# Kernel optimization log

Hardware: AMD Instinct MI355X
Metric: run time of the kernel (lower is better)

Reference implementation:

```python
import jax, jax.numpy as jnp
import numpy as np

# Module hyperparameters (init_kwargs)
KH, KW = 1, 1            # kernel_size
PATCH_H, PATCH_W = 21, 21  # patch_size (displacement grid)
SH, SW = 1, 1            # stride
PAD_H, PAD_W = 0, 0      # padding
DILP_H, DILP_W = 1, 1    # dilation_patch
B, C, H, W = 8, 256, 64, 96


def setup_inputs() -> dict:
    key = jax.random.key(0)
    k1, k2 = jax.random.split(key)
    input1 = jax.random.normal(k1, (B, C, H, W), dtype=jnp.float32)
    input2 = jax.random.normal(k2, (B, C, H, W), dtype=jnp.float32)
    return {"input1": input1, "input2": input2}


def _correlation(x1, x2):
    """FlowNet-style spatial correlation (cost volume).

    out[b, pi, pj, i, j] = sum_{c, ki, kj}
        x1_pad[b, c, i*SH + ki, j*SW + kj] *
        x2_pad[b, c, i*SH + ki + (pi - radH)*DILP_H, j*SW + kj + (pj - radW)*DILP_W]
    Out-of-bounds reads of x2 are zero (handled by padding).
    """
    radH, radW = PATCH_H // 2, PATCH_W // 2
    x1p = jnp.pad(x1, ((0, 0), (0, 0), (PAD_H, PAD_H), (PAD_W, PAD_W)))
    x2p = jnp.pad(x2, ((0, 0), (0, 0),
                       (PAD_H + radH * DILP_H, PAD_H + radH * DILP_H),
                       (PAD_W + radW * DILP_W, PAD_W + radW * DILP_W)))
    Hp, Wp = H + 2 * PAD_H, W + 2 * PAD_W
    oH = (Hp - KH) // SH + 1
    oW = (Wp - KW) // SW + 1

    # displacement grid -> start offsets into x2p (0 corresponds to -rad shift)
    sh = jnp.arange(PATCH_H, dtype=jnp.int32) * DILP_H
    sw = jnp.arange(PATCH_W, dtype=jnp.int32) * DILP_W
    starts = jnp.stack(jnp.meshgrid(sh, sw, indexing="ij"), axis=-1).reshape(-1, 2)

    def step(carry, s):
        # shifted view of x2 aligned with padded x1
        sl = jax.lax.dynamic_slice(x2p, (0, 0, s[0], s[1]), (B, C, Hp, Wp))
        prod = jnp.sum(x1p * sl, axis=1)  # [B, Hp, Wp], channel reduction
        # kernel-window sum + output stride (KH=KW=1 -> single strided slice)
        acc = jnp.zeros((B, oH, oW), dtype=prod.dtype)
        for ki in range(KH):
            for kj in range(KW):
                acc = acc + jax.lax.slice(
                    prod, (0, ki, kj),
                    (B, ki + (oH - 1) * SH + 1, kj + (oW - 1) * SW + 1),
                    (1, SH, SW))
        return carry, acc

    _, out = jax.lax.scan(step, None, starts)  # [PATCH_H*PATCH_W, B, oH, oW]
    out = out.reshape(PATCH_H, PATCH_W, B, oH, oW)
    return jnp.transpose(out, (2, 0, 1, 3, 4))  # [B, patchH, patchW, oH, oW]


def reference(input1, input2):
    return _correlation(input1, input2)
```

## Files before the change

kernel.cpp:

```cpp
#include <hip/hip_runtime.h>

typedef __attribute__((ext_vector_type(8))) short short8;
typedef __attribute__((ext_vector_type(4))) float f32x4;
typedef __attribute__((ext_vector_type(4))) unsigned short us4;

constexpr int NB = 8, NC = 256, IH = 64, IW = 96;
constexpr int PATCH = 21, RAD = 10;
constexpr int TI = 8, TJ = 8;
constexpr int WIN = 28, NWIN = 784;
constexpr int KC = 32, NKS = NC / KC;
constexpr int PLANE = IH * IW;
constexpr int PH = IH + 2 * RAD, PW = IW + 2 * RAD;
constexpr int NBCH = NWIN * 4;
constexpr int NCHUNK = NBCH + 256;
constexpr int ASTR = IH * IW * KC;
constexpr int BSTR = PH * PW * KC;
constexpr size_t X1T_ELEMS = (size_t)NB * NKS * ASTR;
constexpr size_t X2P_ELEMS = (size_t)NB * NKS * BSTR;
constexpr int GSTR = 65;

__device__ __forceinline__ unsigned short f2bf(float f) {
  unsigned u = __builtin_bit_cast(unsigned, f);
  u += 0x7fffu + ((u >> 16) & 1u);
  return (unsigned short)(u >> 16);
}

__global__ __launch_bounds__(256) void x1_to_kmajor(
    const float* __restrict__ src, unsigned short* __restrict__ dst) {
  __shared__ float lsf[32 * 97];
  const int blk = blockIdx.x;
  const int ct = blk & 7, i = (blk >> 3) & 63, b = blk >> 9;
  const int c0 = ct * 32, t = threadIdx.x;
  const float* sp = src + ((size_t)b * NC + c0) * PLANE + (size_t)i * IW;
#pragma unroll
  for (int k = 0; k < 12; ++k) {
    int idx = k * 256 + t;
    int c = idx / 96, j = idx - c * 96;
    lsf[c * 97 + j] = sp[(size_t)c * PLANE + j];
  }
  __syncthreads();
  unsigned short* dp = dst + (((size_t)(b * NKS + ct) * IH + i) * IW) * KC;
#pragma unroll
  for (int k = 0; k < 3; ++k) {
    int o = k * 256 + t;
    int j = o >> 3, cq = o & 7;
    us4 v = {f2bf(lsf[(cq * 4 + 0) * 97 + j]), f2bf(lsf[(cq * 4 + 1) * 97 + j]),
             f2bf(lsf[(cq * 4 + 2) * 97 + j]), f2bf(lsf[(cq * 4 + 3) * 97 + j])};
    *(us4*)&dp[(size_t)j * KC + cq * 4] = v;
  }
}

__global__ __launch_bounds__(256) void x2_to_kmajor_pad(
    const float* __restrict__ src, unsigned short* __restrict__ dst) {
  __shared__ float lsf[32 * 97];
  const int blk = blockIdx.x;
  const int ct = blk & 7, i = (blk >> 3) % PH, b = blk / (PH * 8);
  const int c0 = ct * 32, t = threadIdx.x;
  const int isrc = i - RAD;
  const bool rowok = (unsigned)isrc < (unsigned)IH;
  if (rowok) {
    const float* sp = src + ((size_t)b * NC + c0) * PLANE + (size_t)isrc * IW;
#pragma unroll
    for (int k = 0; k < 12; ++k) {
      int idx = k * 256 + t;
      int c = idx / 96, j = idx - c * 96;
      lsf[c * 97 + j] = sp[(size_t)c * PLANE + j];
    }
  }
  __syncthreads();
  unsigned short* dp = dst + (((size_t)(b * NKS + ct) * PH + i) * PW) * KC;
#pragma unroll
  for (int k = 0; k < 4; ++k) {
    int o = k * 256 + t;
    if (o < PW * 8) {
      int j = o >> 3, cq = o & 7;
      int jsrc = j - RAD;
      us4 v = {0, 0, 0, 0};
      if (rowok && (unsigned)jsrc < (unsigned)IW)
        v = us4{f2bf(lsf[(cq * 4 + 0) * 97 + jsrc]), f2bf(lsf[(cq * 4 + 1) * 97 + jsrc]),
                f2bf(lsf[(cq * 4 + 2) * 97 + jsrc]), f2bf(lsf[(cq * 4 + 3) * 97 + jsrc])};
      *(us4*)&dp[(size_t)j * KC + cq * 4] = v;
    }
  }
}

__global__ __launch_bounds__(512, 2) void corr_pipe8(
    const unsigned short* __restrict__ x1k, const unsigned short* __restrict__ x2k,
    float* __restrict__ out) {
  __shared__ __attribute__((aligned(16))) unsigned short ls[3 * NCHUNK * 8];

  const int t = threadIdx.x, lane = t & 63, wv = t >> 6;
  const int bid = blockIdx.x;
  const int b = bid & 7;
  const int tile = bid >> 3;
  const int ti = tile / 12, tj = tile - ti * 12;
  const int i0 = ti * TI, j0 = tj * TJ;
  const int cbeg = 6 * wv;
  const int qk = lane >> 4, lr = lane & 15;

  const unsigned short* x1b = x1k + (size_t)b * NKS * ASTR;
  const unsigned short* x2b = x2k + (size_t)b * NKS * BSTR;

  const unsigned short* srcp[7];
#pragma unroll
  for (int it = 0; it < 7; ++it) {
    int q = it * 512 + t;
    if (q < NBCH) {
      int w = ((q >> 3) << 1) | (((q >> 2) ^ (q >> 4)) & 1);
      int c4 = (q & 3) ^ (w & 3);
      int wi = w / WIN, wj = w - wi * WIN;
      srcp[it] = x2b + ((size_t)(i0 + wi) * PW + (j0 + wj)) * KC + c4 * 8;
    } else {
      int qa = (q - NBCH) & 255;
      int m = ((qa >> 3) << 1) | (((qa >> 2) ^ (qa >> 4)) & 1);
      int c4 = (qa & 3) ^ (m & 3);
      srcp[it] = x1b + ((size_t)(i0 + (m >> 3)) * IW + (j0 + (m & 7))) * KC + c4 * 8;
    }
  }

  f32x4 acc[4][7];
#pragma unroll
  for (int a = 0; a < 4; ++a)
#pragma unroll
    for (int cc = 0; cc < 7; ++cc) acc[a][cc] = (f32x4){0.f, 0.f, 0.f, 0.f};

#define STAGE(BUF, KS)                                                              \
  {                                                                                 \
    unsigned short* lb = &ls[(BUF) * NCHUNK * 8];                                   \
    _Pragma("unroll")                                                               \
    for (int it = 0; it < 6; ++it)                                                  \
      __builtin_amdgcn_global_load_lds(                                             \
          (const void*)(srcp[it] + (size_t)(KS) * BSTR),                            \
          (void*)(lb + (it * 512 + wv * 64) * 8), 16, 0, 0);                        \
    if (wv < 5)                                                                     \
      __builtin_amdgcn_global_load_lds(                                             \
          (const void*)(srcp[6] + (size_t)(KS) * (wv == 0 ? BSTR : ASTR)),          \
          (void*)(lb + (3072 + wv * 64) * 8), 16, 0, 0);                            \
  }

#define COMPUTE(BUF)                                                                \
  {                                                                                 \
    const unsigned short* lb = &ls[(BUF) * NCHUNK * 8];                             \
    short8 af0 = *(const short8*)(lb + (NBCH + ((4 * (lr) + qk) ^ (lr & 7))) * 8);        \
    short8 af1 = *(const short8*)(lb + (NBCH + ((4 * (16 + lr) + qk) ^ (lr & 7))) * 8);   \
    short8 af2 = *(const short8*)(lb + (NBCH + ((4 * (32 + lr) + qk) ^ (lr & 7))) * 8);   \
    short8 af3 = *(const short8*)(lb + (NBCH + ((4 * (48 + lr) + qk) ^ (lr & 7))) * 8);   \
    _Pragma("unroll")                                                               \
    for (int cc = 0; cc < 7; ++cc) {                                                \
      int wrow = 16 * (cbeg + cc) + lr;                                             \
      int slot = (4 * wrow + qk) ^ (lr & 7);                                        \
      short8 bf = *(const short8*)(lb + slot * 8);                                  \
      acc[0][cc] = __builtin_amdgcn_mfma_f32_16x16x32_bf16(af0, bf, acc[0][cc], 0, 0, 0); \
      acc[1][cc] = __builtin_amdgcn_mfma_f32_16x16x32_bf16(af1, bf, acc[1][cc], 0, 0, 0); \
      acc[2][cc] = __builtin_amdgcn_mfma_f32_16x16x32_bf16(af2, bf, acc[2][cc], 0, 0, 0); \
      acc[3][cc] = __builtin_amdgcn_mfma_f32_16x16x32_bf16(af3, bf, acc[3][cc], 0, 0, 0); \
    }                                                                               \
  }

  STAGE(0, 0)
  STAGE(1, 1)

#define ITER(KS, VM)                                           \
  if ((KS) < 6) STAGE((KS + 2) % 3, KS + 2)                    \
  asm volatile("s_waitcnt vmcnt(" #VM ")" ::: "memory");       \
  asm volatile("s_barrier" ::: "memory");                      \
  COMPUTE(KS % 3)                                              \
  asm volatile("s_barrier" ::: "memory");

  ITER(0, 12)
  ITER(1, 12)
  ITER(2, 12)
  ITER(3, 12)
  ITER(4, 12)
  ITER(5, 12)
  ITER(6, 6)
  ITER(7, 0)
#undef ITER
#undef COMPUTE
#undef STAGE

  float* gf = (float*)ls;
#pragma unroll
  for (int ch = 0; ch < 2; ++ch) {
    __syncthreads();
    const int n0 = ch ? 384 : 0;
#pragma unroll
    for (int a = 0; a < 4; ++a)
#pragma unroll
      for (int cc = 0; cc < 7; ++cc) {
        int ccg = cbeg + cc;
        if (ch ? (ccg >= 24) : (ccg <= 24)) {
          int nl = 16 * ccg + lr - n0;
          int mb = 16 * a + 4 * qk;
          float* gp = &gf[nl * GSTR + mb];
          gp[0] = acc[a][cc][0]; gp[1] = acc[a][cc][1];
          gp[2] = acc[a][cc][2]; gp[3] = acc[a][cc][3];
        }
      }
    __syncthreads();
    for (int s = t; s < 1764; s += 512) {
      int pidx = s / 21, pj = s - pidx * 21;
      int ii = 0, rem = pidx, stop = 0;
#pragma unroll
      for (int k = 0; k < 7; ++k) {
        int cnt = ch ? (7 + k) : (14 - k);
        int go = (!stop) && (rem >= cnt);
        rem -= go ? cnt : 0;
        ii += go;
        stop |= !go;
      }
      int pi = ch ? (14 - ii + rem) : rem;
      int nl = 28 * (pi + ii) + pj - n0;
      int ms = 8 * ii;
      float g[8];
#pragma unroll
      for (int e = 0; e < 8; ++e) g[e] = gf[(nl + e) * GSTR + ms + e];
      float* op = out + ((((size_t)b * PATCH + pi) * PATCH + pj) * IH + (i0 + ii)) * IW + j0;
      f32x4 v0 = {g[0], g[1], g[2], g[3]};
      f32x4 v1 = {g[4], g[5], g[6], g[7]};
      *(f32x4*)op = v0;
      *(f32x4*)(op + 4) = v1;
    }
  }
}

constexpr int LDKF = 40;
__global__ __launch_bounds__(512, 2) void corr_mfma_fb(
    const float* __restrict__ x1, const float* __restrict__ x2, float* __restrict__ out) {
  __shared__ __attribute__((aligned(16))) unsigned short lsA[64 * LDKF];
  __shared__ __attribute__((aligned(16))) unsigned short lsB[NWIN * LDKF];
  const int t = threadIdx.x;
  const int b = blockIdx.y;
  const int ti = blockIdx.x / 12, tj = blockIdx.x % 12;
  const int i0 = ti * TI, j0 = tj * TJ;
  const int lane = t & 63, wv = t >> 6;
  const int mtp = wv >> 2, cg = wv & 3, cbeg = cg * 12;
  const int qk = lane >> 4, lr = lane & 15;
  f32x4 acc[2][13];
#pragma unroll
  for (int a = 0; a < 2; ++a)
#pragma unroll
    for (int cc = 0; cc < 13; ++cc) acc[a][cc] = (f32x4){0.f, 0.f, 0.f, 0.f};
  const int am = t & 63, ak4 = t >> 6;
  const int aii = am >> 3, ajj = am & 7;
  const float* x1p = x1 + ((size_t)b * NC + 4 * ak4) * PLANE + (size_t)(i0 + aii) * IW + (j0 + ajj);
  const float* x2b = x2 + (size_t)b * NC * PLANE;
  for (int ks = 0; ks < NKS; ++ks) {
    __syncthreads();
    {
      const float* p = x1p + (size_t)ks * KC * PLANE;
      us4 v = {f2bf(p[0]), f2bf(p[PLANE]), f2bf(p[2 * PLANE]), f2bf(p[3 * PLANE])};
      *(us4*)&lsA[am * LDKF + 4 * ak4] = v;
    }
    for (int w = t; w < NWIN; w += 512) {
      const int wi = w / WIN, wj = w - wi * WIN;
      const int gi = i0 - RAD + wi, gj = j0 - RAD + wj;
      const bool ok = ((unsigned)gi < (unsigned)IH) && ((unsigned)gj < (unsigned)IW);
      const float* p = x2b + ((size_t)(ks * KC) * IH + gi) * IW + gj;
      unsigned short* dst = &lsB[w * LDKF];
#pragma unroll
      for (int k4 = 0; k4 < 8; ++k4) {
        const float* q = p + (size_t)(4 * k4) * PLANE;
        us4 v = {f2bf(ok ? q[0] : 0.f), f2bf(ok ? q[PLANE] : 0.f),
                 f2bf(ok ? q[2 * PLANE] : 0.f), f2bf(ok ? q[3 * PLANE] : 0.f)};
        *(us4*)&dst[4 * k4] = v;
      }
    }
    __syncthreads();
    short8 a0 = *(const short8*)&lsA[(32 * mtp + lr) * LDKF + 8 * qk];
    short8 a1 = *(const short8*)&lsA[(32 * mtp + 16 + lr) * LDKF + 8 * qk];
#pragma unroll
    for (int cc = 0; cc < 13; ++cc) {
      const int wrow = 16 * (cbeg + cc) + lr;
      short8 bf = *(const short8*)&lsB[wrow * LDKF + 8 * qk];
      acc[0][cc] = __builtin_amdgcn_mfma_f32_16x16x32_bf16(a0, bf, acc[0][cc], 0, 0, 0);
      acc[1][cc] = __builtin_amdgcn_mfma_f32_16x16x32_bf16(a1, bf, acc[1][cc], 0, 0, 0);
    }
  }
#pragma unroll
  for (int a = 0; a < 2; ++a) {
    const int mb = 16 * (2 * mtp + a) + qk * 4;
#pragma unroll
    for (int cc = 0; cc < 13; ++cc) {
      if (cg > 0 && cc == 0) continue;
      const int n = 16 * (cbeg + cc) + lr;
      const int wi = n / WIN, wj = n - wi * WIN;
#pragma unroll
      for (int r = 0; r < 4; ++r) {
        const int m = mb + r;
        const int ii = m >> 3, jj = m & 7;
        const int pi = wi - ii, pj = wj - jj;
        if ((unsigned)pi < (unsigned)PATCH && (unsigned)pj < (unsigned)PATCH)
          out[((((size_t)b * PATCH + pi) * PATCH + pj) * IH + (i0 + ii)) * IW + (j0 + jj)] =
              acc[a][cc][r];
      }
    }
  }
}

extern "C" void kernel_launch(void* const* d_in, const int* in_sizes, int n_in,
                              void* d_out, int out_size, void* d_ws, size_t ws_size,
                              hipStream_t stream) {
  const float* x1 = (const float*)d_in[0];
  const float* x2 = (const float*)d_in[1];
  float* out = (float*)d_out;
  const size_t need = (X1T_ELEMS + X2P_ELEMS) * sizeof(unsigned short);
  if (ws_size >= need) {
    unsigned short* x1k = (unsigned short*)d_ws;
    unsigned short* x2k = x1k + X1T_ELEMS;
    x1_to_kmajor<<<NB * IH * 8, 256, 0, stream>>>(x1, x1k);
    x2_to_kmajor_pad<<<NB * PH * 8, 256, 0, stream>>>(x2, x2k);
    corr_pipe8<<<NB * 96, 512, 0, stream>>>(x1k, x2k, out);
  } else {
    dim3 grid(96, NB);
    corr_mfma_fb<<<grid, 512, 0, stream>>>(x1, x2, out);
  }
}
```

Before: 86.13 us.

## Fuse x1 bf16 conversion into correlation kernel and swizzle epilogue LDS

Drops the separate x1 transpose/convert kernel. The correlation kernel now reads fp32 x1 straight from global memory into registers, converts it to bf16 and writes it to the pipelined LDS buffer, with per-wave vmcnt waits adjusted to match. This removes one launch plus a full write and re-read of x1 in bf16. In exchange, each block now issues strided fp32 loads (each thread reads four channel planes per k-step), and the epilogue LDS staging gets an XOR swizzle to reduce bank conflicts.

Result: no change. 86.39 us (+0.3%).

```diff
diff --git a/kernel.cpp b/kernel.cpp
--- a/kernel.cpp
+++ b/kernel.cpp
@@ -13,9 +13,7 @@
 constexpr int PH = IH + 2 * RAD, PW = IW + 2 * RAD;
 constexpr int NBCH = NWIN * 4;
 constexpr int NCHUNK = NBCH + 256;
-constexpr int ASTR = IH * IW * KC;
 constexpr int BSTR = PH * PW * KC;
-constexpr size_t X1T_ELEMS = (size_t)NB * NKS * ASTR;
 constexpr size_t X2P_ELEMS = (size_t)NB * NKS * BSTR;
 constexpr int GSTR = 65;
 
@@ -23,31 +21,6 @@
   unsigned u = __builtin_bit_cast(unsigned, f);
   u += 0x7fffu + ((u >> 16) & 1u);
   return (unsigned short)(u >> 16);
-}
-
-__global__ __launch_bounds__(256) void x1_to_kmajor(
-    const float* __restrict__ src, unsigned short* __restrict__ dst) {
-  __shared__ float lsf[32 * 97];
-  const int blk = blockIdx.x;
-  const int ct = blk & 7, i = (blk >> 3) & 63, b = blk >> 9;
-  const int c0 = ct * 32, t = threadIdx.x;
-  const float* sp = src + ((size_t)b * NC + c0) * PLANE + (size_t)i * IW;
-#pragma unroll
-  for (int k = 0; k < 12; ++k) {
-    int idx = k * 256 + t;
-    int c = idx / 96, j = idx - c * 96;
-    lsf[c * 97 + j] = sp[(size_t)c * PLANE + j];
-  }
-  __syncthreads();
-  unsigned short* dp = dst + (((size_t)(b * NKS + ct) * IH + i) * IW) * KC;
-#pragma unroll
-  for (int k = 0; k < 3; ++k) {
-    int o = k * 256 + t;
-    int j = o >> 3, cq = o & 7;
-    us4 v = {f2bf(lsf[(cq * 4 + 0) * 97 + j]), f2bf(lsf[(cq * 4 + 1) * 97 + j]),
-             f2bf(lsf[(cq * 4 + 2) * 97 + j]), f2bf(lsf[(cq * 4 + 3) * 97 + j])};
-    *(us4*)&dp[(size_t)j * KC + cq * 4] = v;
-  }
 }
 
 __global__ __launch_bounds__(256) void x2_to_kmajor_pad(
@@ -85,7 +58,7 @@
 }
 
 __global__ __launch_bounds__(512, 2) void corr_pipe8(
-    const unsigned short* __restrict__ x1k, const unsigned short* __restrict__ x2k,
+    const float* __restrict__ x1, const unsigned short* __restrict__ x2k,
     float* __restrict__ out) {
   __shared__ __attribute__((aligned(16))) unsigned short ls[3 * NCHUNK * 8];
 
@@ -98,7 +71,6 @@
   const int cbeg = 6 * wv;
   const int qk = lane >> 4, lr = lane & 15;
 
-  const unsigned short* x1b = x1k + (size_t)b * NKS * ASTR;
   const unsigned short* x2b = x2k + (size_t)b * NKS * BSTR;
 
   const unsigned short* srcp[7];
@@ -111,18 +83,34 @@
       int wi = w / WIN, wj = w - wi * WIN;
       srcp[it] = x2b + ((size_t)(i0 + wi) * PW + (j0 + wj)) * KC + c4 * 8;
     } else {
-      int qa = (q - NBCH) & 255;
-      int m = ((qa >> 3) << 1) | (((qa >> 2) ^ (qa >> 4)) & 1);
-      int c4 = (qa & 3) ^ (m & 3);
-      srcp[it] = x1b + ((size_t)(i0 + (m >> 3)) * IW + (j0 + (m & 7))) * KC + c4 * 8;
-    }
-  }
+      srcp[it] = x2b;
+    }
+  }
+
+  const int am = t & 63, acq = t >> 6;
+  const int aqk = acq >> 1, ah = acq & 1;
+  const float* srcA = x1 + ((size_t)(b * NC) + acq * 4) * PLANE
+                         + (size_t)(i0 + (am >> 3)) * IW + (j0 + (am & 7));
+  const int aoff = (NBCH + ((4 * am + aqk) ^ (am & 7))) * 8 + ah * 4;
 
   f32x4 acc[4][7];
 #pragma unroll
   for (int a = 0; a < 4; ++a)
 #pragma unroll
     for (int cc = 0; cc < 7; ++cc) acc[a][cc] = (f32x4){0.f, 0.f, 0.f, 0.f};
+
+  float fA0, fA1, fA2, fA3, fB0, fB1, fB2, fB3;
+
+#define ALOAD(S, KS)                                                                \
+  {                                                                                 \
+    const float* p = srcA + (size_t)(KS) * KC * PLANE;                              \
+    f##S##0 = p[0]; f##S##1 = p[PLANE]; f##S##2 = p[2 * PLANE]; f##S##3 = p[3 * PLANE]; \
+  }
+#define APACK(S, BUF)                                                               \
+  {                                                                                 \
+    us4 v = {f2bf(f##S##0), f2bf(f##S##1), f2bf(f##S##2), f2bf(f##S##3)};           \
+    *(us4*)&ls[(BUF) * NCHUNK * 8 + aoff] = v;                                      \
+  }
 
 #define STAGE(BUF, KS)                                                              \
   {                                                                                 \
@@ -132,16 +120,16 @@
       __builtin_amdgcn_global_load_lds(                                             \
           (const void*)(srcp[it] + (size_t)(KS) * BSTR),                            \
           (void*)(lb + (it * 512 + wv * 64) * 8), 16, 0, 0);                        \
-    if (wv < 5)                                                                     \
+    if (wv == 0)                                                                    \
       __builtin_amdgcn_global_load_lds(                                             \
-          (const void*)(srcp[6] + (size_t)(KS) * (wv == 0 ? BSTR : ASTR)),          \
-          (void*)(lb + (3072 + wv * 64) * 8), 16, 0, 0);                            \
+          (const void*)(srcp[6] + (size_t)(KS) * BSTR),                             \
+          (void*)(lb + 3072 * 8), 16, 0, 0);                                        \
   }
 
 #define COMPUTE(BUF)                                                                \
   {                                                                                 \
     const unsigned short* lb = &ls[(BUF) * NCHUNK * 8];                             \
-    short8 af0 = *(const short8*)(lb + (NBCH + ((4 * (lr) + qk) ^ (lr & 7))) * 8);        \
+    short8 af0 = *(const short8*)(lb + (NBCH + ((4 * lr + qk) ^ (lr & 7))) * 8);          \
     short8 af1 = *(const short8*)(lb + (NBCH + ((4 * (16 + lr) + qk) ^ (lr & 7))) * 8);   \
     short8 af2 = *(const short8*)(lb + (NBCH + ((4 * (32 + lr) + qk) ^ (lr & 7))) * 8);   \
     short8 af3 = *(const short8*)(lb + (NBCH + ((4 * (48 + lr) + qk) ^ (lr & 7))) * 8);   \
@@ -157,27 +145,40 @@
     }                                                                               \
   }
 
+#define VMW(W0, W)                                                                  \
+  if (wv == 0) { asm volatile("s_waitcnt vmcnt(" #W0 ")" ::: "memory"); }           \
+  else         { asm volatile("s_waitcnt vmcnt(" #W ")" ::: "memory"); }
+
+  ALOAD(A, 0)
   STAGE(0, 0)
+  ALOAD(B, 1)
   STAGE(1, 1)
-
-#define ITER(KS, VM)                                           \
-  if ((KS) < 6) STAGE((KS + 2) % 3, KS + 2)                    \
-  asm volatile("s_waitcnt vmcnt(" #VM ")" ::: "memory");       \
-  asm volatile("s_barrier" ::: "memory");                      \
-  COMPUTE(KS % 3)                                              \
+  VMW(18, 16)
+  APACK(A, 0)
+
+#define ITER(KS, SL, SP, W0, W)                                                     \
+  if ((KS) < 6) { ALOAD(SL, (KS) + 2) STAGE(((KS) + 2) % 3, (KS) + 2) }             \
+  VMW(W0, W)                                                                        \
+  if ((KS) < 7) { APACK(SP, ((KS) + 1) % 3) }                                       \
+  asm volatile("s_waitcnt lgkmcnt(0)" ::: "memory");                                \
+  asm volatile("s_barrier" ::: "memory");                                           \
+  COMPUTE((KS) % 3)                                                                 \
   asm volatile("s_barrier" ::: "memory");
 
-  ITER(0, 12)
-  ITER(1, 12)
-  ITER(2, 12)
-  ITER(3, 12)
-  ITER(4, 12)
-  ITER(5, 12)
-  ITER(6, 6)
-  ITER(7, 0)
+  ITER(0, A, B, 18, 16)
+  ITER(1, B, A, 18, 16)
+  ITER(2, A, B, 18, 16)
+  ITER(3, B, A, 18, 16)
+  ITER(4, A, B, 18, 16)
+  ITER(5, B, A, 18, 16)
+  ITER(6, A, B, 7, 6)
+  ITER(7, B, A, 0, 0)
 #undef ITER
+#undef VMW
 #undef COMPUTE
 #undef STAGE
+#undef APACK
+#undef ALOAD
 
   float* gf = (float*)ls;
 #pragma unroll
@@ -191,8 +192,8 @@
         int ccg = cbeg + cc;
         if (ch ? (ccg >= 24) : (ccg <= 24)) {
           int nl = 16 * ccg + lr - n0;
-          int mb = 16 * a + 4 * qk;
-          float* gp = &gf[nl * GSTR + mb];
+          int sm = 4 * a + qk;
+          float* gp = &gf[nl * GSTR + 4 * (sm ^ (lr & 7))];
           gp[0] = acc[a][cc][0]; gp[1] = acc[a][cc][1];
           gp[2] = acc[a][cc][2]; gp[3] = acc[a][cc][3];
         }
@@ -214,7 +215,10 @@
       int ms = 8 * ii;
       float g[8];
 #pragma unroll
-      for (int e = 0; e < 8; ++e) g[e] = gf[(nl + e) * GSTR + ms + e];
+      for (int e = 0; e < 8; ++e) {
+        int m = ms + e, row = nl + e;
+        g[e] = gf[row * GSTR + 4 * ((m >> 2) ^ (row & 7)) + (m & 3)];
+      }
       float* op = out + ((((size_t)b * PATCH + pi) * PATCH + pj) * IH + (i0 + ii)) * IW + j0;
       f32x4 v0 = {g[0], g[1], g[2], g[3]};
       f32x4 v1 = {g[4], g[5], g[6], g[7]};
@@ -304,13 +308,11 @@
   const float* x1 = (const float*)d_in[0];
   const float* x2 = (const float*)d_in[1];
   float* out = (float*)d_out;
-  const size_t need = (X1T_ELEMS + X2P_ELEMS) * sizeof(unsigned short);
+  const size_t need = X2P_ELEMS * sizeof(unsigned short);
   if (ws_size >= need) {
-    unsigned short* x1k = (unsigned short*)d_ws;
-    unsigned short* x2k = x1k + X1T_ELEMS;
-    x1_to_kmajor<<<NB * IH * 8, 256, 0, stream>>>(x1, x1k);
+    unsigned short* x2k = (unsigned short*)d_ws;
     x2_to_kmajor_pad<<<NB * PH * 8, 256, 0, stream>>>(x2, x2k);
-    corr_pipe8<<<NB * 96, 512, 0, stream>>>(x1k, x2k, out);
+    corr_pipe8<<<NB * 96, 512, 0, stream>>>(x1, x2k, out);
   } else {
     dim3 grid(96, NB);
     corr_mfma_fb<<<grid, 512, 0, stream>>>(x1, x2, out);
```
